# Optimization experiments

Measured on AMD Instinct MI355X. Metric: run time of the kernel, lower is better.

## Reference

```python
import jax, jax.numpy as jnp
import numpy as np

EPS = 1e-6


def setup_inputs() -> dict:
    key = jax.random.key(0)
    k1, k2, k3 = jax.random.split(key, 3)
    B, H, L, D = 1, 16, 1024, 64
    return {
        "q": jax.random.normal(k1, (B, H, L, D), dtype=jnp.float32),
        "k": jax.random.normal(k2, (B, H, L, D), dtype=jnp.float32),
        "v": jax.random.normal(k3, (B, H, L, D), dtype=jnp.float32),
    }


def reference(q, k, v):
    bsz, head_num, tgt_len, dim = q.shape
    src_len = k.shape[2]
    m = max(src_len, tgt_len)

    # flatten batch*heads: [N, L, D]
    q = jax.nn.relu(q.reshape(-1, tgt_len, dim))
    k = jax.nn.relu(k.reshape(-1, src_len, dim))
    v = v.reshape(-1, src_len, dim)

    # cosFormer re-weighting index: pi/2 * (1..m) / m, shape [1, m, 1]
    idx = (np.pi / 2) * jnp.arange(1, m + 1, dtype=q.dtype).reshape(1, -1, 1) / m
    sin_w = jnp.sin(idx)
    cos_w = jnp.cos(idx)

    # feature-mapped q/k: [N, L, 2D]
    q_ = jnp.concatenate([q * sin_w[:, :tgt_len, :], q * cos_w[:, :tgt_len, :]], axis=-1)
    k_ = jnp.concatenate([k * sin_w[:, :src_len, :], k * cos_w[:, :src_len, :]], axis=-1)

    # causal linear attention via cumulative outer products
    kv_ = jnp.einsum("nld,nlm->nldm", k_, v)          # [N, L, 2D, D]
    kv_cum = jnp.cumsum(kv_, axis=1)
    qkv = jnp.einsum("nld,nldm->nlm", q_, kv_cum)      # [N, L, D]

    k_cum = jnp.cumsum(k_, axis=1)                      # [N, L, 2D]
    denom = jnp.clip(jnp.einsum("nld,nld->nl", q_, k_cum), EPS, None)

    out = qkv / denom[..., None]
    return out.reshape(bsz, head_num, tgt_len, dim)
```

## Files before the change

kernel.cpp:

```cpp
#include <hip/hip_runtime.h>

namespace {
constexpr int Hh = 16;
constexpr int Ll = 1024;
constexpr int Dd = 64;
constexpr int Cc = 64;
constexpr int NCHUNK = Ll / Cc;
constexpr float PI_HALF = 1.5707963267948966f;
constexpr float EPSV = 1e-6f;
constexpr int KV_ELEMS = 64 * 128;
constexpr size_t KV_TOTAL_E = (size_t)Hh * NCHUNK * KV_ELEMS;
}

typedef __attribute__((ext_vector_type(8))) short short8;
typedef __attribute__((ext_vector_type(4))) float floatx4;

__device__ __forceinline__ unsigned short f2bf(float x) {
    unsigned int u = __float_as_uint(x);
    unsigned int r = u + 0x7fffu + ((u >> 16) & 1u);
    return (unsigned short)(r >> 16);
}
__device__ __forceinline__ float bf2f(unsigned short b) {
    return __uint_as_float(((unsigned int)b) << 16);
}

#define MFMA16(a, b, c) __builtin_amdgcn_mfma_f32_16x16x32_bf16((a), (b), (c), 0, 0, 0)

__global__ __launch_bounds__(512)
void cf_sums(const float* __restrict__ kin, const float* __restrict__ vin,
             unsigned short* __restrict__ wskv, unsigned short* __restrict__ wsks) {
    const int c = blockIdx.x, h = blockIdx.y;
    const int tid = threadIdx.x;
    constexpr int S1 = 72, SC = 136;
    __shared__ unsigned short Ak[128 * S1];
    __shared__ unsigned short Bv1[80 * S1];
    __shared__ unsigned short Cst[64 * SC];
    __shared__ unsigned short Ks[128];

    const size_t gbase = ((size_t)h * Ll + (size_t)c * Cc) * Dd;
    const float4* k4 = (const float4*)(kin + gbase);
    const float4* v4 = (const float4*)(vin + gbase);
    #pragma unroll
    for (int i = 0; i < 2; ++i) {
        int e4 = i * 512 + tid;
        int j = e4 >> 4, d4 = (e4 & 15) * 4;
        float th = PI_HALF * (float)(c * Cc + j + 1) * (1.0f / (float)Ll);
        float sj, cj; __sincosf(th, &sj, &cj);
        float4 kx = k4[e4];
        float r0 = fmaxf(kx.x, 0.f), r1 = fmaxf(kx.y, 0.f);
        float r2 = fmaxf(kx.z, 0.f), r3 = fmaxf(kx.w, 0.f);
        Ak[(d4 + 0) * S1 + j] = f2bf(r0 * sj);
        Ak[(d4 + 1) * S1 + j] = f2bf(r1 * sj);
        Ak[(d4 + 2) * S1 + j] = f2bf(r2 * sj);
        Ak[(d4 + 3) * S1 + j] = f2bf(r3 * sj);
        Ak[(64 + d4 + 0) * S1 + j] = f2bf(r0 * cj);
        Ak[(64 + d4 + 1) * S1 + j] = f2bf(r1 * cj);
        Ak[(64 + d4 + 2) * S1 + j] = f2bf(r2 * cj);
        Ak[(64 + d4 + 3) * S1 + j] = f2bf(r3 * cj);
        float4 vx = v4[e4];
        Bv1[(d4 + 0) * S1 + j] = f2bf(vx.x);
        Bv1[(d4 + 1) * S1 + j] = f2bf(vx.y);
        Bv1[(d4 + 2) * S1 + j] = f2bf(vx.z);
        Bv1[(d4 + 3) * S1 + j] = f2bf(vx.w);
    }
    if (tid < 64) Bv1[64 * S1 + tid] = 0x3F80;
    if (tid >= 64 && tid < 72) Bv1[64 * S1 + tid] = 0;
    {
        int z = tid;
        if (z < 540) ((unsigned int*)Bv1)[(65 * S1) / 2 + z] = 0u;
        z = 512 + tid;
        if (z < 540) ((unsigned int*)Bv1)[(65 * S1) / 2 + z] = 0u;
    }
    __syncthreads();

    const int wave = tid >> 6, lane = tid & 63;
    const int lrow = lane & 15, quad = lane >> 4;
    {
        const int ft = wave;
        short8 af[2];
        #pragma unroll
        for (int ks = 0; ks < 2; ++ks)
            af[ks] = *(const short8*)&Ak[(ft * 16 + lrow) * S1 + ks * 32 + quad * 8];
        #pragma unroll
        for (int nt = 0; nt < 5; ++nt) {
            floatx4 acc = {0.f, 0.f, 0.f, 0.f};
            #pragma unroll
            for (int ks = 0; ks < 2; ++ks) {
                short8 bf = *(const short8*)&Bv1[(nt * 16 + lrow) * S1 + ks * 32 + quad * 8];
                acc = MFMA16(af[ks], bf, acc);
            }
            ushort4 pk = make_ushort4(f2bf(acc[0]), f2bf(acc[1]), f2bf(acc[2]), f2bf(acc[3]));
            if (nt < 4) {
                *(ushort4*)&Cst[(nt * 16 + lrow) * SC + ft * 16 + quad * 4] = pk;
            } else if (lrow == 0) {
                *(ushort4*)&Ks[ft * 16 + quad * 4] = pk;
            }
        }
    }
    __syncthreads();

    unsigned short* kvout = wskv + (size_t)(h * NCHUNK + c) * KV_ELEMS;
    #pragma unroll
    for (int i = 0; i < 2; ++i) {
        int idx = i * 512 + tid;
        int row = idx >> 4, c8 = (idx & 15) * 8;
        *(uint4*)(kvout + row * 128 + c8) = *(const uint4*)&Cst[row * SC + c8];
    }
    if (tid < 16)
        *(uint4*)(wsks + (size_t)(h * NCHUNK + c) * 128 + tid * 8) =
            *(const uint4*)&Ks[tid * 8];
}

__global__ __launch_bounds__(256)
void cf_scan(unsigned short* __restrict__ wskv, unsigned short* __restrict__ wsks) {
    const int bx = blockIdx.x, h = blockIdx.y;
    const int tid = threadIdx.x;
    if (bx < 32) {
        unsigned short* p = wskv + (size_t)h * NCHUNK * KV_ELEMS + bx * 256 + tid;
        unsigned short vals[NCHUNK];
        #pragma unroll
        for (int cc = 0; cc < NCHUNK; ++cc)
            vals[cc] = p[(size_t)cc * KV_ELEMS];
        float run = 0.f;
        #pragma unroll
        for (int cc = 0; cc < NCHUNK; ++cc) {
            p[(size_t)cc * KV_ELEMS] = f2bf(run);
            run += bf2f(vals[cc]);
        }
    } else if (tid < 128) {
        unsigned short* p = wsks + (size_t)h * NCHUNK * 128 + tid;
        unsigned short vals[NCHUNK];
        #pragma unroll
        for (int cc = 0; cc < NCHUNK; ++cc)
            vals[cc] = p[cc * 128];
        float run = 0.f;
        #pragma unroll
        for (int cc = 0; cc < NCHUNK; ++cc) {
            p[cc * 128] = f2bf(run);
            run += bf2f(vals[cc]);
        }
    }
}

__global__ __launch_bounds__(512)
void cf_out(const float* __restrict__ qin, const float* __restrict__ kin,
            const float* __restrict__ vin,
            const unsigned short* __restrict__ wskv,
            const unsigned short* __restrict__ wsks,
            float* __restrict__ out) {
    const int c = blockIdx.x, h = blockIdx.y;
    const int tid = threadIdx.x;
    constexpr int SA = 200, SB = 136, SV = 200;
    __shared__ unsigned short Aq[64 * SA];
    __shared__ unsigned short Bk[80 * SB];
    __shared__ unsigned short Bv[64 * SV];

    const int wave = tid >> 6, lane = tid & 63;
    const int lrow = lane & 15, quad = lane >> 4;

    const uint4* s4g = (const uint4*)(wskv + (size_t)(h * NCHUNK + c) * KV_ELEMS);
    uint4 sreg0 = s4g[tid];
    uint4 sreg1 = s4g[512 + tid];
    uint4 kreg;
    if (tid < 16)
        kreg = ((const uint4*)(wsks + (size_t)(h * NCHUNK + c) * 128))[tid];

    {
        int z = tid;
        if (z < 1020) ((unsigned int*)Bk)[(65 * SB) / 2 + z] = 0u;
        z = 512 + tid;
        if (z < 1020) ((unsigned int*)Bk)[(65 * SB) / 2 + z] = 0u;
    }

    const size_t gbase = ((size_t)h * Ll + (size_t)c * Cc) * Dd;
    const float4* q4 = (const float4*)(qin + gbase);
    const float4* k4 = (const float4*)(kin + gbase);
    const float4* v4 = (const float4*)(vin + gbase);
    #pragma unroll
    for (int i = 0; i < 2; ++i) {
        int e4 = i * 512 + tid;
        int j = e4 >> 4, d4 = (e4 & 15) * 4;
        float th = PI_HALF * (float)(c * Cc + j + 1) * (1.0f / (float)Ll);
        float sj, cj; __sincosf(th, &sj, &cj);
        float4 qv = q4[e4];
        float q0 = fmaxf(qv.x, 0.f), q1 = fmaxf(qv.y, 0.f);
        float q2 = fmaxf(qv.z, 0.f), q3 = fmaxf(qv.w, 0.f);
        *(ushort4*)&Aq[j * SA + 64 + d4] =
            make_ushort4(f2bf(q0 * sj), f2bf(q1 * sj), f2bf(q2 * sj), f2bf(q3 * sj));
        *(ushort4*)&Aq[j * SA + 128 + d4] =
            make_ushort4(f2bf(q0 * cj), f2bf(q1 * cj), f2bf(q2 * cj), f2bf(q3 * cj));
        float4 kx = k4[e4];
        float k0 = fmaxf(kx.x, 0.f), k1 = fmaxf(kx.y, 0.f);
        float k2 = fmaxf(kx.z, 0.f), k3 = fmaxf(kx.w, 0.f);
        *(ushort4*)&Bk[j * SB + d4] =
            make_ushort4(f2bf(k0 * sj), f2bf(k1 * sj), f2bf(k2 * sj), f2bf(k3 * sj));
        *(ushort4*)&Bk[j * SB + 64 + d4] =
            make_ushort4(f2bf(k0 * cj), f2bf(k1 * cj), f2bf(k2 * cj), f2bf(k3 * cj));
        float4 vx = v4[e4];
        Bv[(d4 + 0) * SV + j] = f2bf(vx.x);
        Bv[(d4 + 1) * SV + j] = f2bf(vx.y);
        Bv[(d4 + 2) * SV + j] = f2bf(vx.z);
        Bv[(d4 + 3) * SV + j] = f2bf(vx.w);
    }
    {
        int idx = tid;
        *(uint4*)&Bv[(idx >> 4) * SV + 64 + (idx & 15) * 8] = sreg0;
        idx = 512 + tid;
        *(uint4*)&Bv[(idx >> 4) * SV + 64 + (idx & 15) * 8] = sreg1;
        if (tid < 16) *(uint4*)&Bk[64 * SB + tid * 8] = kreg;
    }
    __syncthreads();

    const int l0 = wave * 16;
    const int arow = (l0 + lrow) * SA;
    short8 a1f[4];
    float inv[4];

    if (wave < 4) {
        #pragma unroll
        for (int ks = 0; ks < 4; ++ks)
            a1f[ks] = *(const short8*)&Aq[arow + 64 + ks * 32 + quad * 8];
        floatx4 rs = {0.f, 0.f, 0.f, 0.f};
        #pragma unroll
        for (int nt = 0; nt < 5; ++nt) {
            floatx4 sc = {0.f, 0.f, 0.f, 0.f};
            #pragma unroll
            for (int ks = 0; ks < 4; ++ks) {
                short8 bf = *(const short8*)&Bk[(nt * 16 + lrow) * SB + ks * 32 + quad * 8];
                sc = MFMA16(a1f[ks], bf, sc);
            }
            if (nt < 4) {
                int j = nt * 16 + lrow;
                #pragma unroll
                for (int r = 0; r < 4; ++r) {
                    int l = l0 + quad * 4 + r;
                    float m = (j <= l) ? sc[r] : 0.f;
                    sc[r] = m;
                    Aq[l * SA + j] = f2bf(m);
                }
            }
            rs += sc;
        }
        #pragma unroll
        for (int m = 1; m <= 8; m <<= 1) {
            rs[0] += __shfl_xor(rs[0], m);
            rs[1] += __shfl_xor(rs[1], m);
            rs[2] += __shfl_xor(rs[2], m);
            rs[3] += __shfl_xor(rs[3], m);
        }
        #pragma unroll
        for (int r = 0; r < 4; ++r) inv[r] = 1.0f / fmaxf(rs[r], EPSV);
    }
    __syncthreads();

    if (wave < 4) {
        short8 sc0 = *(const short8*)&Aq[arow + 0 * 32 + quad * 8];
        short8 sc1 = *(const short8*)&Aq[arow + 1 * 32 + quad * 8];
        #pragma unroll
        for (int nt = 0; nt < 4; ++nt) {
            const int brow = (nt * 16 + lrow) * SV;
            floatx4 oacc = {0.f, 0.f, 0.f, 0.f};
            short8 b0 = *(const short8*)&Bv[brow + 0 * 32 + quad * 8];
            oacc = MFMA16(sc0, b0, oacc);
            short8 b1 = *(const short8*)&Bv[brow + 1 * 32 + quad * 8];
            oacc = MFMA16(sc1, b1, oacc);
            #pragma unroll
            for (int ks = 2; ks < 6; ++ks) {
                short8 bf = *(const short8*)&Bv[brow + ks * 32 + quad * 8];
                oacc = MFMA16(a1f[ks - 2], bf, oacc);
            }
            #pragma unroll
            for (int r = 0; r < 4; ++r) {
                int l = l0 + quad * 4 + r;
                out[gbase + (size_t)l * Dd + nt * 16 + lrow] = oacc[r] * inv[r];
            }
        }
    }
}

extern "C" void kernel_launch(void* const* d_in, const int* in_sizes, int n_in,
                              void* d_out, int out_size, void* d_ws, size_t ws_size,
                              hipStream_t stream) {
    const float* q = (const float*)d_in[0];
    const float* k = (const float*)d_in[1];
    const float* v = (const float*)d_in[2];
    float* out = (float*)d_out;
    unsigned short* wskv = (unsigned short*)d_ws;
    unsigned short* wsks = wskv + KV_TOTAL_E;
    dim3 grid(NCHUNK, Hh);
    cf_sums<<<grid, 512, 0, stream>>>(k, v, wskv, wsks);
    cf_scan<<<dim3(33, Hh), 256, 0, stream>>>(wskv, wsks);
    cf_out<<<grid, 512, 0, stream>>>(q, k, v, wskv, wsks, out);
}
```

Baseline: 74.92 us.

## Fuse chunk prefix scan into output kernel, removing separate scan launch

Drops the standalone cf_scan kernel. Each output block now sums the per-chunk KV and K-sum states of all preceding chunks directly from the workspace, in batches of five with register accumulation. This saves one kernel launch and the workspace read-modify-write pass. In exchange, later chunks do redundant work that grows with the chunk index (up to 15 state reads per block), which unbalances the load. The q/k/v loads are also moved earlier so their latency overlaps with the prefix reduction.

```diff
diff --git a/kernel.cpp b/kernel.cpp
--- a/kernel.cpp
+++ b/kernel.cpp
@@ -111,43 +111,12 @@
             *(const uint4*)&Ks[tid * 8];
 }
 
-__global__ __launch_bounds__(256)
-void cf_scan(unsigned short* __restrict__ wskv, unsigned short* __restrict__ wsks) {
-    const int bx = blockIdx.x, h = blockIdx.y;
-    const int tid = threadIdx.x;
-    if (bx < 32) {
-        unsigned short* p = wskv + (size_t)h * NCHUNK * KV_ELEMS + bx * 256 + tid;
-        unsigned short vals[NCHUNK];
-        #pragma unroll
-        for (int cc = 0; cc < NCHUNK; ++cc)
-            vals[cc] = p[(size_t)cc * KV_ELEMS];
-        float run = 0.f;
-        #pragma unroll
-        for (int cc = 0; cc < NCHUNK; ++cc) {
-            p[(size_t)cc * KV_ELEMS] = f2bf(run);
-            run += bf2f(vals[cc]);
-        }
-    } else if (tid < 128) {
-        unsigned short* p = wsks + (size_t)h * NCHUNK * 128 + tid;
-        unsigned short vals[NCHUNK];
-        #pragma unroll
-        for (int cc = 0; cc < NCHUNK; ++cc)
-            vals[cc] = p[cc * 128];
-        float run = 0.f;
-        #pragma unroll
-        for (int cc = 0; cc < NCHUNK; ++cc) {
-            p[cc * 128] = f2bf(run);
-            run += bf2f(vals[cc]);
-        }
-    }
-}
-
 __global__ __launch_bounds__(512)
-void cf_out(const float* __restrict__ qin, const float* __restrict__ kin,
-            const float* __restrict__ vin,
-            const unsigned short* __restrict__ wskv,
-            const unsigned short* __restrict__ wsks,
-            float* __restrict__ out) {
+void cf_out2b(const float* __restrict__ qin, const float* __restrict__ kin,
+              const float* __restrict__ vin,
+              const unsigned short* __restrict__ wskv,
+              const unsigned short* __restrict__ wsks,
+              float* __restrict__ out) {
     const int c = blockIdx.x, h = blockIdx.y;
     const int tid = threadIdx.x;
     constexpr int SA = 200, SB = 136, SV = 200;
@@ -158,12 +127,46 @@
     const int wave = tid >> 6, lane = tid & 63;
     const int lrow = lane & 15, quad = lane >> 4;
 
-    const uint4* s4g = (const uint4*)(wskv + (size_t)(h * NCHUNK + c) * KV_ELEMS);
-    uint4 sreg0 = s4g[tid];
-    uint4 sreg1 = s4g[512 + tid];
-    uint4 kreg;
-    if (tid < 16)
-        kreg = ((const uint4*)(wsks + (size_t)(h * NCHUNK + c) * 128))[tid];
+    const size_t gbase = ((size_t)h * Ll + (size_t)c * Cc) * Dd;
+    const float4* q4 = (const float4*)(qin + gbase);
+    const float4* k4 = (const float4*)(kin + gbase);
+    const float4* v4 = (const float4*)(vin + gbase);
+    float4 qr[2], kr[2], vr[2];
+    qr[0] = q4[tid]; qr[1] = q4[512 + tid];
+    kr[0] = k4[tid]; kr[1] = k4[512 + tid];
+    vr[0] = v4[tid]; vr[1] = v4[512 + tid];
+
+    float facc[16];
+    #pragma unroll
+    for (int e = 0; e < 16; ++e) facc[e] = 0.f;
+    const unsigned short* sb = wskv + (size_t)h * NCHUNK * KV_ELEMS + tid * 16;
+    for (int base = 0; base < c; base += 5) {
+        uint4 r0[5], r1[5];
+        #pragma unroll
+        for (int b = 0; b < 5; ++b) {
+            if (base + b < c) {
+                const unsigned short* p = sb + (size_t)(base + b) * KV_ELEMS;
+                r0[b] = *(const uint4*)p;
+                r1[b] = *(const uint4*)(p + 8);
+            }
+        }
+        #pragma unroll
+        for (int b = 0; b < 5; ++b) {
+            if (base + b < c) {
+                const unsigned short* u0 = (const unsigned short*)&r0[b];
+                const unsigned short* u1 = (const unsigned short*)&r1[b];
+                #pragma unroll
+                for (int e = 0; e < 8; ++e) facc[e] += bf2f(u0[e]);
+                #pragma unroll
+                for (int e = 0; e < 8; ++e) facc[8 + e] += bf2f(u1[e]);
+            }
+        }
+    }
+    float kacc = 0.f;
+    if (tid < 128) {
+        const unsigned short* kb = wsks + (size_t)h * NCHUNK * 128 + tid;
+        for (int cc = 0; cc < c; ++cc) kacc += bf2f(kb[cc * 128]);
+    }
 
     {
         int z = tid;
@@ -172,42 +175,41 @@
         if (z < 1020) ((unsigned int*)Bk)[(65 * SB) / 2 + z] = 0u;
     }
 
-    const size_t gbase = ((size_t)h * Ll + (size_t)c * Cc) * Dd;
-    const float4* q4 = (const float4*)(qin + gbase);
-    const float4* k4 = (const float4*)(kin + gbase);
-    const float4* v4 = (const float4*)(vin + gbase);
     #pragma unroll
     for (int i = 0; i < 2; ++i) {
         int e4 = i * 512 + tid;
         int j = e4 >> 4, d4 = (e4 & 15) * 4;
         float th = PI_HALF * (float)(c * Cc + j + 1) * (1.0f / (float)Ll);
         float sj, cj; __sincosf(th, &sj, &cj);
-        float4 qv = q4[e4];
+        float4 qv = qr[i];
         float q0 = fmaxf(qv.x, 0.f), q1 = fmaxf(qv.y, 0.f);
         float q2 = fmaxf(qv.z, 0.f), q3 = fmaxf(qv.w, 0.f);
         *(ushort4*)&Aq[j * SA + 64 + d4] =
             make_ushort4(f2bf(q0 * sj), f2bf(q1 * sj), f2bf(q2 * sj), f2bf(q3 * sj));
         *(ushort4*)&Aq[j * SA + 128 + d4] =
             make_ushort4(f2bf(q0 * cj), f2bf(q1 * cj), f2bf(q2 * cj), f2bf(q3 * cj));
-        float4 kx = k4[e4];
+        float4 kx = kr[i];
         float k0 = fmaxf(kx.x, 0.f), k1 = fmaxf(kx.y, 0.f);
         float k2 = fmaxf(kx.z, 0.f), k3 = fmaxf(kx.w, 0.f);
         *(ushort4*)&Bk[j * SB + d4] =
             make_ushort4(f2bf(k0 * sj), f2bf(k1 * sj), f2bf(k2 * sj), f2bf(k3 * sj));
         *(ushort4*)&Bk[j * SB + 64 + d4] =
             make_ushort4(f2bf(k0 * cj), f2bf(k1 * cj), f2bf(k2 * cj), f2bf(k3 * cj));
-        float4 vx = v4[e4];
+        float4 vx = vr[i];
         Bv[(d4 + 0) * SV + j] = f2bf(vx.x);
         Bv[(d4 + 1) * SV + j] = f2bf(vx.y);
         Bv[(d4 + 2) * SV + j] = f2bf(vx.z);
         Bv[(d4 + 3) * SV + j] = f2bf(vx.w);
     }
     {
-        int idx = tid;
-        *(uint4*)&Bv[(idx >> 4) * SV + 64 + (idx & 15) * 8] = sreg0;
-        idx = 512 + tid;
-        *(uint4*)&Bv[(idx >> 4) * SV + 64 + (idx & 15) * 8] = sreg1;
-        if (tid < 16) *(uint4*)&Bk[64 * SB + tid * 8] = kreg;
+        const int d = tid >> 3, f0 = (tid & 7) * 16;
+        #pragma unroll
+        for (int e4i = 0; e4i < 4; ++e4i) {
+            *(ushort4*)&Bv[d * SV + 64 + f0 + e4i * 4] =
+                make_ushort4(f2bf(facc[e4i * 4 + 0]), f2bf(facc[e4i * 4 + 1]),
+                             f2bf(facc[e4i * 4 + 2]), f2bf(facc[e4i * 4 + 3]));
+        }
+        if (tid < 128) Bk[64 * SB + tid] = f2bf(kacc);
     }
     __syncthreads();
 
@@ -289,6 +291,5 @@
     unsigned short* wsks = wskv + KV_TOTAL_E;
     dim3 grid(NCHUNK, Hh);
     cf_sums<<<grid, 512, 0, stream>>>(k, v, wskv, wsks);
-    cf_scan<<<dim3(33, Hh), 256, 0, stream>>>(wskv, wsks);
-    cf_out<<<grid, 512, 0, stream>>>(q, k, v, wskv, wsks, out);
-}
+    cf_out2b<<<grid, 512, 0, stream>>>(q, k, v, wskv, wsks, out);
+}
```

New measurement: 78.11 us. 1.04x slower.
